# Optimization experiments

Hardware: AMD Instinct MI355X
Metric: run time of the kernel (lower is better)

Reference implementation:

```python
import jax, jax.numpy as jnp
import numpy as np

N, D, E, H, O, K = 4096, 1024, 8, 2048, 1024, 2
LOSS_COEF = 0.01


def setup_inputs() -> dict:
    key = jax.random.key(0)
    ks = jax.random.split(key, 8)
    x = jax.random.normal(ks[0], (N, D), jnp.float32)
    return {
        "x": x,
        "x_offsets": jnp.array([0, N // 2, N], jnp.int32),  # unused by forward math
        "max_seq_len": 2048,
        "group_norm": False,
        "num_groups": 8,
        "linear_dim": D // 8,
        "norm_weight": jax.random.uniform(ks[1], (D,), jnp.float32, 0.5, 1.5),
        "norm_bias": jax.random.normal(ks[2], (D,), jnp.float32) * 0.1,
        "norm_eps": 1e-5,
        "w_gate": jax.random.normal(ks[3], (D, E), jnp.float32) * (1.0 / np.sqrt(D)),
        "experts_hidden_w": jax.random.normal(ks[4], (E, H, D), jnp.float32) * 0.02,
        "experts_hidden_bias": jnp.zeros((E, H), jnp.float32),
        "experts_w": jax.random.normal(ks[5], (E, O, H), jnp.float32) * 0.02,
        "experts_bias": jnp.zeros((E, O), jnp.float32),
        "output_weight": jax.random.normal(ks[6], (D, O), jnp.float32) * 0.02,
    }


def _cv_squared(v, eps=1e-6):
    v = v.astype(jnp.float32)
    m = v.mean()
    return jnp.var(v, ddof=1) / (m * m + eps)  # torch .var() is unbiased


def reference(x, x_offsets, max_seq_len, group_norm, num_groups, linear_dim,
              norm_weight, norm_bias, norm_eps,
              w_gate, experts_hidden_w, experts_hidden_bias,
              experts_w, experts_bias, output_weight):
    # ---- input normalization (layer_norm branch; group_norm=False) ----
    if group_norm:
        xg = x.reshape(-1, num_groups, linear_dim)
        mu = xg.mean(axis=2, keepdims=True)
        var = ((xg - mu) ** 2).mean(axis=2, keepdims=True)
        xg = (xg - mu) * jax.lax.rsqrt(var + norm_eps)
        xg = xg * norm_weight[None, :, None] + norm_bias[None, :, None]
        x_norm = xg.reshape(-1, x.shape[-1])
    else:
        mu = x.mean(axis=-1, keepdims=True)
        var = ((x - mu) ** 2).mean(axis=-1, keepdims=True)  # biased, like F.layer_norm
        x_norm = (x - mu) * jax.lax.rsqrt(var + norm_eps) * norm_weight + norm_bias

    # ---- gating: clean logits (enable_noisy_gating=False), L2-normalize rows ----
    logits = x_norm @ w_gate                                  # [N, E]
    logits = logits / jnp.maximum(
        jnp.linalg.norm(logits, axis=1, keepdims=True), 1e-12)
    probs = jax.nn.softmax(logits, axis=1)                    # softmax over all experts
    _, top_idx = jax.lax.top_k(logits, K)                     # [N, K]
    gates_k = jnp.take_along_axis(probs, top_idx, axis=1)     # top-k of softmax(logits)
    rows = jnp.arange(logits.shape[0])[:, None]
    gates = jnp.zeros_like(logits).at[rows, top_idx].set(gates_k)  # [N, E] sparse gates

    # ---- load-balancing loss (train=True, non-noisy path) ----
    importance = gates.sum(axis=0)
    load = (gates > 0).sum(axis=0).astype(jnp.float32)
    loss = (_cv_squared(importance) + _cv_squared(load)) * LOSS_COEF

    # ---- expert MLPs; gates are exactly zero off top-k so masked-dense == dispatch ----
    h = jax.nn.silu(jnp.einsum('nd,ehd->enh', x_norm, experts_hidden_w)
                    + experts_hidden_bias[:, None, :])        # [E, N, H]
    eo = jnp.einsum('enh,eoh->eno', h, experts_w) + experts_bias[:, None, :]  # [E, N, O]
    y_moe = jnp.einsum('ne,eno->no', gates.astype(jnp.float32),
                       eo.astype(jnp.float32))                # fp32 combine, like index_add

    # ---- residual projection: addmm(y_moe, x, output_weight) ----
    y = y_moe + x @ output_weight
    gate_fraction = load / load.sum()
    return (y, loss, gate_fraction)
```

## Files before the change

### kernel.cpp

```cpp
#include <hip/hip_runtime.h>
#include <hip/hip_bf16.h>
#include <stdint.h>

#define N_TOK 4096
#define DIM   1024
#define NE    8
#define NH    2048
#define NO    1024

typedef __attribute__((ext_vector_type(8))) short bf16x8;
typedef __attribute__((ext_vector_type(16))) float f32x16;

__device__ inline unsigned short f2bf(float f) {
    unsigned u = __float_as_uint(f);
    u += 0x7fffu + ((u >> 16) & 1u);
    return (unsigned short)(u >> 16);
}

__device__ inline void async_copy16(const void* g, void* l) {
    __builtin_amdgcn_global_load_lds(
        (const __attribute__((address_space(1))) void*)g,
        (__attribute__((address_space(3))) void*)l, 16, 0, 0);
}

__global__ __launch_bounds__(256) void ln_gate_kernel(
    const float* __restrict__ x, const float* __restrict__ nw,
    const float* __restrict__ nb, const float* __restrict__ eps_p,
    const float* __restrict__ wg,
    unsigned short* __restrict__ xn_bf, unsigned short* __restrict__ x_bf,
    int* __restrict__ tok_e, float* __restrict__ tok_g)
{
    int n = blockIdx.x;
    int t = threadIdx.x;
    int lane = t & 63, wv = t >> 6;

    const float4 xv = ((const float4*)(x + (size_t)n * DIM))[t];
    float s  = xv.x + xv.y + xv.z + xv.w;
    float s2 = xv.x*xv.x + xv.y*xv.y + xv.z*xv.z + xv.w*xv.w;
    #pragma unroll
    for (int o = 32; o > 0; o >>= 1) {
        s  += __shfl_down(s, o);
        s2 += __shfl_down(s2, o);
    }
    __shared__ float rs[4], rs2[4];
    __shared__ float gred[4][NE];
    if (lane == 0) { rs[wv] = s; rs2[wv] = s2; }
    __syncthreads();
    float S  = rs[0] + rs[1] + rs[2] + rs[3];
    float S2 = rs2[0] + rs2[1] + rs2[2] + rs2[3];
    const float inv = 1.0f / (float)DIM;
    float mu = S * inv;
    float var = fmaxf(S2 * inv - mu * mu, 0.0f);
    float rstd = rsqrtf(var + eps_p[0]);

    float4 w4 = ((const float4*)nw)[t];
    float4 b4 = ((const float4*)nb)[t];
    float xn0 = (xv.x - mu) * rstd * w4.x + b4.x;
    float xn1 = (xv.y - mu) * rstd * w4.y + b4.y;
    float xn2 = (xv.z - mu) * rstd * w4.z + b4.z;
    float xn3 = (xv.w - mu) * rstd * w4.w + b4.w;

    ushort4 pn; pn.x = f2bf(xn0); pn.y = f2bf(xn1); pn.z = f2bf(xn2); pn.w = f2bf(xn3);
    ((ushort4*)(xn_bf + (size_t)n * DIM))[t] = pn;
    ushort4 px; px.x = f2bf(xv.x); px.y = f2bf(xv.y); px.z = f2bf(xv.z); px.w = f2bf(xv.w);
    ((ushort4*)(x_bf + (size_t)n * DIM))[t] = px;

    float acc[NE];
    #pragma unroll
    for (int e = 0; e < NE; ++e) acc[e] = 0.0f;
    float xns[4] = {xn0, xn1, xn2, xn3};
    const float4* wgp = (const float4*)(wg + (size_t)(4 * t) * NE);
    #pragma unroll
    for (int j = 0; j < 4; ++j) {
        float4 w0 = wgp[2 * j], w1 = wgp[2 * j + 1];
        float xj = xns[j];
        acc[0] += xj * w0.x; acc[1] += xj * w0.y; acc[2] += xj * w0.z; acc[3] += xj * w0.w;
        acc[4] += xj * w1.x; acc[5] += xj * w1.y; acc[6] += xj * w1.z; acc[7] += xj * w1.w;
    }
    #pragma unroll
    for (int o = 32; o > 0; o >>= 1) {
        #pragma unroll
        for (int e = 0; e < NE; ++e) acc[e] += __shfl_down(acc[e], o);
    }
    if (lane == 0) {
        #pragma unroll
        for (int e = 0; e < NE; ++e) gred[wv][e] = acc[e];
    }
    __syncthreads();
    if (t == 0) {
        float lg[NE];
        float nrm2 = 0.0f;
        #pragma unroll
        for (int e = 0; e < NE; ++e) {
            lg[e] = gred[0][e] + gred[1][e] + gred[2][e] + gred[3][e];
            nrm2 += lg[e] * lg[e];
        }
        float den = fmaxf(sqrtf(nrm2), 1e-12f);
        float linv = 1.0f / den;
        #pragma unroll
        for (int e = 0; e < NE; ++e) lg[e] *= linv;
        float mx = lg[0];
        #pragma unroll
        for (int e = 1; e < NE; ++e) mx = fmaxf(mx, lg[e]);
        float p[NE], ps = 0.0f;
        #pragma unroll
        for (int e = 0; e < NE; ++e) { p[e] = expf(lg[e] - mx); ps += p[e]; }
        float pinv = 1.0f / ps;
        #pragma unroll
        for (int e = 0; e < NE; ++e) p[e] *= pinv;
        int i0 = 0; float b0 = lg[0];
        #pragma unroll
        for (int e = 1; e < NE; ++e) if (lg[e] > b0) { b0 = lg[e]; i0 = e; }
        int i1 = -1; float b1 = -3.0e38f;
        #pragma unroll
        for (int e = 0; e < NE; ++e) if (e != i0 && lg[e] > b1) { b1 = lg[e]; i1 = e; }
        tok_e[2 * n] = i0; tok_e[2 * n + 1] = i1;
        tok_g[2 * n] = p[i0]; tok_g[2 * n + 1] = p[i1];
    }
}

__device__ inline float cv_sq(const float* v) {
    float m = 0.0f;
    for (int e = 0; e < NE; ++e) m += v[e];
    m *= (1.0f / NE);
    float s = 0.0f;
    for (int e = 0; e < NE; ++e) { float d = v[e] - m; s += d * d; }
    s *= (1.0f / (NE - 1));
    return s / (m * m + 1e-6f);
}

#define CVT_BLK 32768
__global__ __launch_bounds__(256) void prep_kernel(
    const float* __restrict__ whw, unsigned short* __restrict__ wh_bf,
    const float* __restrict__ wow, unsigned short* __restrict__ wo_bf,
    const float* __restrict__ wout, unsigned short* __restrict__ wt_bf,
    const int* __restrict__ tok_e, const float* __restrict__ tok_g,
    int* __restrict__ counts, int* __restrict__ offsets,
    int* __restrict__ rowsbuf, float* __restrict__ gatebuf,
    float* __restrict__ out_tail)
{
    __shared__ float tile[32][33];
    __shared__ int   sc[4][NE], sp[4][NE];
    __shared__ float sf[4][NE];
    __shared__ int   lcur[NE];

    int b = blockIdx.x, t = threadIdx.x;

    if (b < CVT_BLK) {
        const int n4each = NE * NH * DIM / 4;
        int i = b * 256 + t;
        const float4* s; ushort4* d; int j;
        if (i < n4each) { s = (const float4*)whw; d = (ushort4*)wh_bf; j = i; }
        else            { s = (const float4*)wow; d = (ushort4*)wo_bf; j = i - n4each; }
        float4 v = s[j];
        ushort4 o; o.x = f2bf(v.x); o.y = f2bf(v.y); o.z = f2bf(v.z); o.w = f2bf(v.w);
        d[j] = o;
        return;
    }
    if (b < CVT_BLK + 1024) {
        int idx = b - CVT_BLK;
        int o0 = (idx & 31) * 32, d0 = (idx >> 5) * 32;
        int tx = t & 31, ty0 = t >> 5;
        #pragma unroll
        for (int k = 0; k < 4; ++k) {
            int ty = ty0 + k * 8;
            tile[ty][tx] = wout[(size_t)(d0 + ty) * NO + o0 + tx];
        }
        __syncthreads();
        #pragma unroll
        for (int k = 0; k < 4; ++k) {
            int ty = ty0 + k * 8;
            wt_bf[(size_t)(o0 + ty) * DIM + d0 + tx] = f2bf(tile[tx][ty]);
        }
        return;
    }

    int rb = b - (CVT_BLK + 1024);
    int lane = t & 63, wv = t >> 6;
    int chunk0 = rb * 1024;

    int lc[NE]; float li[NE];
    #pragma unroll
    for (int e = 0; e < NE; ++e) { lc[e] = 0; li[e] = 0.0f; }
    int base = t * 32;
    #pragma unroll
    for (int q = 0; q < 8; ++q) {
        int4 e4 = *(const int4*)(tok_e + base + q * 4);
        float4 g4 = *(const float4*)(tok_g + base + q * 4);
        lc[e4.x]++; li[e4.x] += g4.x;
        lc[e4.y]++; li[e4.y] += g4.y;
        lc[e4.z]++; li[e4.z] += g4.z;
        lc[e4.w]++; li[e4.w] += g4.w;
    }
    int prior_flag = (base + 32 <= chunk0) ? 1 : 0;
    int lp[NE];
    #pragma unroll
    for (int e = 0; e < NE; ++e) lp[e] = prior_flag ? lc[e] : 0;

    #pragma unroll
    for (int o = 32; o > 0; o >>= 1) {
        #pragma unroll
        for (int e = 0; e < NE; ++e) {
            lc[e] += __shfl_down(lc[e], o);
            lp[e] += __shfl_down(lp[e], o);
            li[e] += __shfl_down(li[e], o);
        }
    }
    if (lane == 0) {
        #pragma unroll
        for (int e = 0; e < NE; ++e) { sc[wv][e] = lc[e]; sp[wv][e] = lp[e]; sf[wv][e] = li[e]; }
    }
    __syncthreads();
    if (t == 0) {
        int cnt[NE], pri[NE]; float imp[NE];
        for (int e = 0; e < NE; ++e) {
            cnt[e] = sc[0][e] + sc[1][e] + sc[2][e] + sc[3][e];
            pri[e] = sp[0][e] + sp[1][e] + sp[2][e] + sp[3][e];
            imp[e] = sf[0][e] + sf[1][e] + sf[2][e] + sf[3][e];
        }
        int off = 0;
        for (int e = 0; e < NE; ++e) {
            lcur[e] = off + pri[e];
            if (rb == 0) { counts[e] = cnt[e]; offsets[e] = off; }
            off += cnt[e];
        }
        if (rb == 0) {
            float lcf[NE], lif[NE];
            for (int e = 0; e < NE; ++e) { lcf[e] = (float)cnt[e]; lif[e] = imp[e]; }
            float tot = (float)off;
            out_tail[0] = 0.01f * (cv_sq(lif) + cv_sq(lcf));
            for (int e = 0; e < NE; ++e) out_tail[1 + e] = lcf[e] / tot;
        }
    }
    __syncthreads();

    int g0 = chunk0 + 4 * t;
    int4 e4 = *(const int4*)(tok_e + g0);
    float4 g4 = *(const float4*)(tok_g + g0);
    int s0 = atomicAdd(&lcur[e4.x], 1);
    int s1 = atomicAdd(&lcur[e4.y], 1);
    int s2 = atomicAdd(&lcur[e4.z], 1);
    int s3 = atomicAdd(&lcur[e4.w], 1);
    int tok0 = g0 >> 1;
    rowsbuf[s0] = tok0;     rowsbuf[s1] = tok0;
    rowsbuf[s2] = tok0 + 1; rowsbuf[s3] = tok0 + 1;
    gatebuf[s0] = g4.x; gatebuf[s1] = g4.y;
    gatebuf[s2] = g4.z; gatebuf[s3] = g4.w;
}

#define BK 64

__global__ __launch_bounds__(256) void gemm1_kernel(
    const unsigned short* __restrict__ xn,
    const unsigned short* __restrict__ wh,
    const float* __restrict__ hb,
    const int* __restrict__ rowsbuf,
    const int* __restrict__ counts, const int* __restrict__ offsets,
    unsigned short* __restrict__ hbuf)
{
    int e = blockIdx.z;
    int count = counts[e];
    int tm = blockIdx.y, tn = blockIdx.x;
    if (tm * 128 >= count) return;
    int off = offsets[e];

    __shared__ alignas(16) short As[128 * BK];
    __shared__ alignas(16) short Bs[128 * BK];

    int t = threadIdx.x;
    int c = t & 7, rl = t >> 3;
    int csw = (c ^ (rl & 7)) * 8;
    const unsigned short* aptr[4];
    const unsigned short* bptr[4];
    #pragma unroll
    for (int p = 0; p < 4; ++p) {
        int mrow = tm * 128 + p * 32 + rl;
        int mc = mrow < count ? mrow : count - 1;
        int token = rowsbuf[off + mc];
        aptr[p] = xn + (size_t)token * DIM;
        bptr[p] = wh + ((size_t)e * NH + tn * 128 + p * 32 + rl) * DIM;
    }

    int lane = t & 63, wvi = t >> 6;
    int wm = (wvi & 1) * 64, wn = (wvi >> 1) * 64;
    int l31 = lane & 31, h = lane >> 5, sw = l31 & 7;

    f32x16 acc[2][2];
    #pragma unroll
    for (int i = 0; i < 2; ++i)
        #pragma unroll
        for (int j = 0; j < 2; ++j) acc[i][j] = (f32x16)(0.0f);

    for (int kt = 0; kt < DIM / BK; ++kt) {
        int kb = kt * BK + csw;
        #pragma unroll
        for (int p = 0; p < 4; ++p)
            async_copy16(aptr[p] + kb, (char*)As + p * 4096 + t * 16);
        #pragma unroll
        for (int p = 0; p < 4; ++p)
            async_copy16(bptr[p] + kb, (char*)Bs + p * 4096 + t * 16);
        __syncthreads();
        #pragma unroll
        for (int ks = 0; ks < 4; ++ks) {
            int ph = ((ks * 2 + h) ^ sw) * 8;
            bf16x8 af[2], bfr[2];
            #pragma unroll
            for (int i = 0; i < 2; ++i)
                af[i] = *(const bf16x8*)&As[(wm + i * 32 + l31) * BK + ph];
            #pragma unroll
            for (int j = 0; j < 2; ++j)
                bfr[j] = *(const bf16x8*)&Bs[(wn + j * 32 + l31) * BK + ph];
            #pragma unroll
            for (int i = 0; i < 2; ++i)
                #pragma unroll
                for (int j = 0; j < 2; ++j)
                    acc[i][j] = __builtin_amdgcn_mfma_f32_32x32x16_bf16(af[i], bfr[j], acc[i][j], 0, 0, 0);
        }
        __syncthreads();
    }

    #pragma unroll
    for (int i = 0; i < 2; ++i) {
        #pragma unroll
        for (int j = 0; j < 2; ++j) {
            int col = tn * 128 + wn + j * 32 + l31;
            float bias = hb[e * NH + col];
            #pragma unroll
            for (int r = 0; r < 16; ++r) {
                int row_d = (r & 3) + 8 * (r >> 2) + 4 * h;
                int m = tm * 128 + wm + i * 32 + row_d;
                if (m < count) {
                    float v = acc[i][j][r] + bias;
                    v = v / (1.0f + __expf(-v));
                    hbuf[(size_t)(off + m) * NH + col] = f2bf(v);
                }
            }
        }
    }
}

__global__ __launch_bounds__(256) void gemm2_kernel(
    const unsigned short* __restrict__ hbuf,
    const unsigned short* __restrict__ wo,
    const float* __restrict__ ob,
    const int* __restrict__ counts, const int* __restrict__ offsets,
    const int* __restrict__ rowsbuf, const float* __restrict__ gatebuf,
    float* __restrict__ y)
{
    int e = blockIdx.z;
    int count = counts[e];
    int tm = blockIdx.y, tn = blockIdx.x;
    if (tm * 128 >= count) return;
    int off = offsets[e];

    __shared__ alignas(16) short As[128 * BK];
    __shared__ alignas(16) short Bs[64 * BK];

    int t = threadIdx.x;
    int c = t & 7, rl = t >> 3;
    int csw = (c ^ (rl & 7)) * 8;
    const unsigned short* aptr[4];
    const unsigned short* bptr[2];
    #pragma unroll
    for (int p = 0; p < 4; ++p) {
        int mrow = tm * 128 + p * 32 + rl;
        int mc = mrow < count ? mrow : count - 1;
        aptr[p] = hbuf + (size_t)(off + mc) * NH;
    }
    #pragma unroll
    for (int p = 0; p < 2; ++p)
        bptr[p] = wo + ((size_t)e * NO + tn * 64 + p * 32 + rl) * NH;

    int lane = t & 63, wvi = t >> 6;
    int wm = (wvi & 1) * 64, wn = (wvi >> 1) * 32;
    int l31 = lane & 31, h = lane >> 5, sw = l31 & 7;

    f32x16 acc[2];
    #pragma unroll
    for (int i = 0; i < 2; ++i) acc[i] = (f32x16)(0.0f);

    for (int kt = 0; kt < NH / BK; ++kt) {
        int kb = kt * BK + csw;
        #pragma unroll
        for (int p = 0; p < 4; ++p)
            async_copy16(aptr[p] + kb, (char*)As + p * 4096 + t * 16);
        #pragma unroll
        for (int p = 0; p < 2; ++p)
            async_copy16(bptr[p] + kb, (char*)Bs + p * 4096 + t * 16);
        __syncthreads();
        #pragma unroll
        for (int ks = 0; ks < 4; ++ks) {
            int ph = ((ks * 2 + h) ^ sw) * 8;
            bf16x8 af[2], bfr;
            #pragma unroll
            for (int i = 0; i < 2; ++i)
                af[i] = *(const bf16x8*)&As[(wm + i * 32 + l31) * BK + ph];
            bfr = *(const bf16x8*)&Bs[(wn + l31) * BK + ph];
            #pragma unroll
            for (int i = 0; i < 2; ++i)
                acc[i] = __builtin_amdgcn_mfma_f32_32x32x16_bf16(af[i], bfr, acc[i], 0, 0, 0);
        }
        __syncthreads();
    }

    int col = tn * 64 + wn + l31;
    float bias = ob[e * NO + col];
    #pragma unroll
    for (int i = 0; i < 2; ++i) {
        #pragma unroll
        for (int r = 0; r < 16; ++r) {
            int row_d = (r & 3) + 8 * (r >> 2) + 4 * h;
            int m = tm * 128 + wm + i * 32 + row_d;
            if (m < count) {
                int slot = off + m;
                int token = rowsbuf[slot];
                float g = gatebuf[slot];
                __hip_atomic_fetch_add(&y[(size_t)token * NO + col],
                                       g * (acc[i][r] + bias),
                                       __ATOMIC_RELAXED, __HIP_MEMORY_SCOPE_AGENT);
            }
        }
    }
}

__global__ __launch_bounds__(256) void gemm_res_kernel(
    const unsigned short* __restrict__ xb,
    const unsigned short* __restrict__ wt,
    float* __restrict__ y)
{
    int tm = blockIdx.y, tn = blockIdx.x;
    __shared__ alignas(16) short As[64 * BK];
    __shared__ alignas(16) short Bs[128 * BK];

    int t = threadIdx.x;
    int c = t & 7, rl = t >> 3;
    int csw = (c ^ (rl & 7)) * 8;
    const unsigned short* aptr[2];
    const unsigned short* bptr[4];
    #pragma unroll
    for (int p = 0; p < 2; ++p)
        aptr[p] = xb + (size_t)(tm * 64 + p * 32 + rl) * DIM;
    #pragma unroll
    for (int p = 0; p < 4; ++p)
        bptr[p] = wt + (size_t)(tn * 128 + p * 32 + rl) * DIM;

    int lane = t & 63, wvi = t >> 6;
    int wm = (wvi & 1) * 32, wn = (wvi >> 1) * 64;
    int l31 = lane & 31, h = lane >> 5, sw = l31 & 7;

    f32x16 acc[2];
    #pragma unroll
    for (int j = 0; j < 2; ++j) acc[j] = (f32x16)(0.0f);

    for (int kt = 0; kt < DIM / BK; ++kt) {
        int kb = kt * BK + csw;
        #pragma unroll
        for (int p = 0; p < 2; ++p)
            async_copy16(aptr[p] + kb, (char*)As + p * 4096 + t * 16);
        #pragma unroll
        for (int p = 0; p < 4; ++p)
            async_copy16(bptr[p] + kb, (char*)Bs + p * 4096 + t * 16);
        __syncthreads();
        #pragma unroll
        for (int ks = 0; ks < 4; ++ks) {
            int ph = ((ks * 2 + h) ^ sw) * 8;
            bf16x8 af, bfr[2];
            af = *(const bf16x8*)&As[(wm + l31) * BK + ph];
            #pragma unroll
            for (int j = 0; j < 2; ++j)
                bfr[j] = *(const bf16x8*)&Bs[(wn + j * 32 + l31) * BK + ph];
            #pragma unroll
            for (int j = 0; j < 2; ++j)
                acc[j] = __builtin_amdgcn_mfma_f32_32x32x16_bf16(af, bfr[j], acc[j], 0, 0, 0);
        }
        __syncthreads();
    }

    #pragma unroll
    for (int j = 0; j < 2; ++j) {
        int col = tn * 128 + wn + j * 32 + l31;
        #pragma unroll
        for (int r = 0; r < 16; ++r) {
            int row_d = (r & 3) + 8 * (r >> 2) + 4 * h;
            int row = tm * 64 + wm + row_d;
            y[(size_t)row * NO + col] = acc[j][r];
        }
    }
}

extern "C" void kernel_launch(void* const* d_in, const int* in_sizes, int n_in,
                              void* d_out, int out_size, void* d_ws, size_t ws_size,
                              hipStream_t stream) {
    const float* x    = (const float*)d_in[0];
    const float* nw   = (const float*)d_in[6];
    const float* nb   = (const float*)d_in[7];
    const float* eps  = (const float*)d_in[8];
    const float* wg   = (const float*)d_in[9];
    const float* whw  = (const float*)d_in[10];
    const float* whb  = (const float*)d_in[11];
    const float* wow  = (const float*)d_in[12];
    const float* wob  = (const float*)d_in[13];
    const float* wout = (const float*)d_in[14];

    char* ws = (char*)d_ws;
    unsigned short* xn_bf = (unsigned short*)(ws + 0);
    unsigned short* x_bf  = (unsigned short*)(ws + 8388608);
    unsigned short* wh_bf = (unsigned short*)(ws + 16777216);
    unsigned short* wo_bf = (unsigned short*)(ws + 50331648);
    unsigned short* wt_bf = (unsigned short*)(ws + 83886080);
    unsigned short* hbuf  = (unsigned short*)(ws + 85983232);
    char* meta = ws + 119537664;
    int*   counts     = (int*)(meta + 0);
    int*   offsets    = (int*)(meta + 128);
    int*   tok_e      = (int*)(meta + 2048);
    float* tok_g      = (float*)(meta + 2048 + 32768);
    int*   rowsbuf    = (int*)(meta + 2048 + 65536);
    float* gatebuf    = (float*)(meta + 2048 + 98304);

    float* y = (float*)d_out;
    float* out_tail = y + (size_t)N_TOK * NO;

    ln_gate_kernel<<<N_TOK, 256, 0, stream>>>(x, nw, nb, eps, wg, xn_bf, x_bf,
                                              tok_e, tok_g);
    prep_kernel<<<CVT_BLK + 1024 + 8, 256, 0, stream>>>(
        whw, wh_bf, wow, wo_bf, wout, wt_bf,
        tok_e, tok_g, counts, offsets, rowsbuf, gatebuf, out_tail);
    gemm_res_kernel<<<dim3(NO / 128, N_TOK / 64), 256, 0, stream>>>(x_bf, wt_bf, y);
    gemm1_kernel<<<dim3(NH / 128, N_TOK / 128, NE), 256, 0, stream>>>(
        xn_bf, wh_bf, whb, rowsbuf, counts, offsets, hbuf);
    gemm2_kernel<<<dim3(NO / 64, N_TOK / 128, NE), 256, 0, stream>>>(
        hbuf, wo_bf, wob, counts, offsets, rowsbuf, gatebuf, y);
}
```

Baseline: 382.9 us.

## Replace atomic MoE scatter with gather-combine in residual GEMM epilogue

```diff
diff --git a/kernel.cpp b/kernel.cpp
--- a/kernel.cpp
+++ b/kernel.cpp
@@ -23,99 +23,138 @@
         (__attribute__((address_space(3))) void*)l, 16, 0, 0);
 }
 
-__global__ __launch_bounds__(256) void ln_gate_kernel(
+#define LN_BLK  4096
+#define CVT_BLK 32768
+__global__ __launch_bounds__(256) void fused_prep_kernel(
     const float* __restrict__ x, const float* __restrict__ nw,
     const float* __restrict__ nb, const float* __restrict__ eps_p,
     const float* __restrict__ wg,
     unsigned short* __restrict__ xn_bf, unsigned short* __restrict__ x_bf,
-    int* __restrict__ tok_e, float* __restrict__ tok_g)
+    int* __restrict__ tok_e, float* __restrict__ tok_g,
+    const float* __restrict__ whw, unsigned short* __restrict__ wh_bf,
+    const float* __restrict__ wow, unsigned short* __restrict__ wo_bf,
+    const float* __restrict__ wout, unsigned short* __restrict__ wt_bf)
 {
-    int n = blockIdx.x;
-    int t = threadIdx.x;
-    int lane = t & 63, wv = t >> 6;
-
-    const float4 xv = ((const float4*)(x + (size_t)n * DIM))[t];
-    float s  = xv.x + xv.y + xv.z + xv.w;
-    float s2 = xv.x*xv.x + xv.y*xv.y + xv.z*xv.z + xv.w*xv.w;
-    #pragma unroll
-    for (int o = 32; o > 0; o >>= 1) {
-        s  += __shfl_down(s, o);
-        s2 += __shfl_down(s2, o);
-    }
+    __shared__ float tile[32][33];
     __shared__ float rs[4], rs2[4];
     __shared__ float gred[4][NE];
-    if (lane == 0) { rs[wv] = s; rs2[wv] = s2; }
+
+    int b = blockIdx.x, t = threadIdx.x;
+
+    if (b < LN_BLK) {
+        int n = b;
+        int lane = t & 63, wv = t >> 6;
+
+        const float4 xv = ((const float4*)(x + (size_t)n * DIM))[t];
+        float s  = xv.x + xv.y + xv.z + xv.w;
+        float s2 = xv.x*xv.x + xv.y*xv.y + xv.z*xv.z + xv.w*xv.w;
+        #pragma unroll
+        for (int o = 32; o > 0; o >>= 1) {
+            s  += __shfl_down(s, o);
+            s2 += __shfl_down(s2, o);
+        }
+        if (lane == 0) { rs[wv] = s; rs2[wv] = s2; }
+        __syncthreads();
+        float S  = rs[0] + rs[1] + rs[2] + rs[3];
+        float S2 = rs2[0] + rs2[1] + rs2[2] + rs2[3];
+        const float inv = 1.0f / (float)DIM;
+        float mu = S * inv;
+        float var = fmaxf(S2 * inv - mu * mu, 0.0f);
+        float rstd = rsqrtf(var + eps_p[0]);
+
+        float4 w4 = ((const float4*)nw)[t];
+        float4 b4 = ((const float4*)nb)[t];
+        float xn0 = (xv.x - mu) * rstd * w4.x + b4.x;
+        float xn1 = (xv.y - mu) * rstd * w4.y + b4.y;
+        float xn2 = (xv.z - mu) * rstd * w4.z + b4.z;
+        float xn3 = (xv.w - mu) * rstd * w4.w + b4.w;
+
+        ushort4 pn; pn.x = f2bf(xn0); pn.y = f2bf(xn1); pn.z = f2bf(xn2); pn.w = f2bf(xn3);
+        ((ushort4*)(xn_bf + (size_t)n * DIM))[t] = pn;
+        ushort4 px; px.x = f2bf(xv.x); px.y = f2bf(xv.y); px.z = f2bf(xv.z); px.w = f2bf(xv.w);
+        ((ushort4*)(x_bf + (size_t)n * DIM))[t] = px;
+
+        float acc[NE];
+        #pragma unroll
+        for (int e = 0; e < NE; ++e) acc[e] = 0.0f;
+        float xns[4] = {xn0, xn1, xn2, xn3};
+        const float4* wgp = (const float4*)(wg + (size_t)(4 * t) * NE);
+        #pragma unroll
+        for (int j = 0; j < 4; ++j) {
+            float4 w0 = wgp[2 * j], w1 = wgp[2 * j + 1];
+            float xj = xns[j];
+            acc[0] += xj * w0.x; acc[1] += xj * w0.y; acc[2] += xj * w0.z; acc[3] += xj * w0.w;
+            acc[4] += xj * w1.x; acc[5] += xj * w1.y; acc[6] += xj * w1.z; acc[7] += xj * w1.w;
+        }
+        #pragma unroll
+        for (int o = 32; o > 0; o >>= 1) {
+            #pragma unroll
+            for (int e = 0; e < NE; ++e) acc[e] += __shfl_down(acc[e], o);
+        }
+        if (lane == 0) {
+            #pragma unroll
+            for (int e = 0; e < NE; ++e) gred[wv][e] = acc[e];
+        }
+        __syncthreads();
+        if (t == 0) {
+            float lg[NE];
+            float nrm2 = 0.0f;
+            #pragma unroll
+            for (int e = 0; e < NE; ++e) {
+                lg[e] = gred[0][e] + gred[1][e] + gred[2][e] + gred[3][e];
+                nrm2 += lg[e] * lg[e];
+            }
+            float den = fmaxf(sqrtf(nrm2), 1e-12f);
+            float linv = 1.0f / den;
+            #pragma unroll
+            for (int e = 0; e < NE; ++e) lg[e] *= linv;
+            float mx = lg[0];
+            #pragma unroll
+            for (int e = 1; e < NE; ++e) mx = fmaxf(mx, lg[e]);
+            float p[NE], ps = 0.0f;
+            #pragma unroll
+            for (int e = 0; e < NE; ++e) { p[e] = expf(lg[e] - mx); ps += p[e]; }
+            float pinv = 1.0f / ps;
+            #pragma unroll
+            for (int e = 0; e < NE; ++e) p[e] *= pinv;
+            int i0 = 0; float b0 = lg[0];
+            #pragma unroll
+            for (int e = 1; e < NE; ++e) if (lg[e] > b0) { b0 = lg[e]; i0 = e; }
+            int i1 = -1; float b1 = -3.0e38f;
+            #pragma unroll
+            for (int e = 0; e < NE; ++e) if (e != i0 && lg[e] > b1) { b1 = lg[e]; i1 = e; }
+            tok_e[2 * n] = i0; tok_e[2 * n + 1] = i1;
+            tok_g[2 * n] = p[i0]; tok_g[2 * n + 1] = p[i1];
+        }
+        return;
+    }
+
+    int b2 = b - LN_BLK;
+    if (b2 < CVT_BLK) {
+        const int n4each = NE * NH * DIM / 4;
+        int i = b2 * 256 + t;
+        const float4* s; ushort4* d; int j;
+        if (i < n4each) { s = (const float4*)whw; d = (ushort4*)wh_bf; j = i; }
+        else            { s = (const float4*)wow; d = (ushort4*)wo_bf; j = i - n4each; }
+        float4 v = s[j];
+        ushort4 o; o.x = f2bf(v.x); o.y = f2bf(v.y); o.z = f2bf(v.z); o.w = f2bf(v.w);
+        d[j] = o;
+        return;
+    }
+
+    int idx = b2 - CVT_BLK;
+    int o0 = (idx & 31) * 32, d0 = (idx >> 5) * 32;
+    int tx = t & 31, ty0 = t >> 5;
+    #pragma unroll
+    for (int k = 0; k < 4; ++k) {
+        int ty = ty0 + k * 8;
+        tile[ty][tx] = wout[(size_t)(d0 + ty) * NO + o0 + tx];
+    }
     __syncthreads();
-    float S  = rs[0] + rs[1] + rs[2] + rs[3];
-    float S2 = rs2[0] + rs2[1] + rs2[2] + rs2[3];
-    const float inv = 1.0f / (float)DIM;
-    float mu = S * inv;
-    float var = fmaxf(S2 * inv - mu * mu, 0.0f);
-    float rstd = rsqrtf(var + eps_p[0]);
-
-    float4 w4 = ((const float4*)nw)[t];
-    float4 b4 = ((const float4*)nb)[t];
-    float xn0 = (xv.x - mu) * rstd * w4.x + b4.x;
-    float xn1 = (xv.y - mu) * rstd * w4.y + b4.y;
-    float xn2 = (xv.z - mu) * rstd * w4.z + b4.z;
-    float xn3 = (xv.w - mu) * rstd * w4.w + b4.w;
-
-    ushort4 pn; pn.x = f2bf(xn0); pn.y = f2bf(xn1); pn.z = f2bf(xn2); pn.w = f2bf(xn3);
-    ((ushort4*)(xn_bf + (size_t)n * DIM))[t] = pn;
-    ushort4 px; px.x = f2bf(xv.x); px.y = f2bf(xv.y); px.z = f2bf(xv.z); px.w = f2bf(xv.w);
-    ((ushort4*)(x_bf + (size_t)n * DIM))[t] = px;
-
-    float acc[NE];
-    #pragma unroll
-    for (int e = 0; e < NE; ++e) acc[e] = 0.0f;
-    float xns[4] = {xn0, xn1, xn2, xn3};
-    const float4* wgp = (const float4*)(wg + (size_t)(4 * t) * NE);
-    #pragma unroll
-    for (int j = 0; j < 4; ++j) {
-        float4 w0 = wgp[2 * j], w1 = wgp[2 * j + 1];
-        float xj = xns[j];
-        acc[0] += xj * w0.x; acc[1] += xj * w0.y; acc[2] += xj * w0.z; acc[3] += xj * w0.w;
-        acc[4] += xj * w1.x; acc[5] += xj * w1.y; acc[6] += xj * w1.z; acc[7] += xj * w1.w;
-    }
-    #pragma unroll
-    for (int o = 32; o > 0; o >>= 1) {
-        #pragma unroll
-        for (int e = 0; e < NE; ++e) acc[e] += __shfl_down(acc[e], o);
-    }
-    if (lane == 0) {
-        #pragma unroll
-        for (int e = 0; e < NE; ++e) gred[wv][e] = acc[e];
-    }
-    __syncthreads();
-    if (t == 0) {
-        float lg[NE];
-        float nrm2 = 0.0f;
-        #pragma unroll
-        for (int e = 0; e < NE; ++e) {
-            lg[e] = gred[0][e] + gred[1][e] + gred[2][e] + gred[3][e];
-            nrm2 += lg[e] * lg[e];
-        }
-        float den = fmaxf(sqrtf(nrm2), 1e-12f);
-        float linv = 1.0f / den;
-        #pragma unroll
-        for (int e = 0; e < NE; ++e) lg[e] *= linv;
-        float mx = lg[0];
-        #pragma unroll
-        for (int e = 1; e < NE; ++e) mx = fmaxf(mx, lg[e]);
-        float p[NE], ps = 0.0f;
-        #pragma unroll
-        for (int e = 0; e < NE; ++e) { p[e] = expf(lg[e] - mx); ps += p[e]; }
-        float pinv = 1.0f / ps;
-        #pragma unroll
-        for (int e = 0; e < NE; ++e) p[e] *= pinv;
-        int i0 = 0; float b0 = lg[0];
-        #pragma unroll
-        for (int e = 1; e < NE; ++e) if (lg[e] > b0) { b0 = lg[e]; i0 = e; }
-        int i1 = -1; float b1 = -3.0e38f;
-        #pragma unroll
-        for (int e = 0; e < NE; ++e) if (e != i0 && lg[e] > b1) { b1 = lg[e]; i1 = e; }
-        tok_e[2 * n] = i0; tok_e[2 * n + 1] = i1;
-        tok_g[2 * n] = p[i0]; tok_g[2 * n + 1] = p[i1];
+    #pragma unroll
+    for (int k = 0; k < 4; ++k) {
+        int ty = ty0 + k * 8;
+        wt_bf[(size_t)(o0 + ty) * DIM + d0 + tx] = f2bf(tile[tx][ty]);
     }
 }
 
@@ -129,53 +168,17 @@
     return s / (m * m + 1e-6f);
 }
 
-#define CVT_BLK 32768
-__global__ __launch_bounds__(256) void prep_kernel(
-    const float* __restrict__ whw, unsigned short* __restrict__ wh_bf,
-    const float* __restrict__ wow, unsigned short* __restrict__ wo_bf,
-    const float* __restrict__ wout, unsigned short* __restrict__ wt_bf,
+__global__ __launch_bounds__(256) void routing_kernel(
     const int* __restrict__ tok_e, const float* __restrict__ tok_g,
     int* __restrict__ counts, int* __restrict__ offsets,
-    int* __restrict__ rowsbuf, float* __restrict__ gatebuf,
+    int* __restrict__ rowsbuf, int* __restrict__ invslot,
     float* __restrict__ out_tail)
 {
-    __shared__ float tile[32][33];
     __shared__ int   sc[4][NE], sp[4][NE];
     __shared__ float sf[4][NE];
     __shared__ int   lcur[NE];
 
-    int b = blockIdx.x, t = threadIdx.x;
-
-    if (b < CVT_BLK) {
-        const int n4each = NE * NH * DIM / 4;
-        int i = b * 256 + t;
-        const float4* s; ushort4* d; int j;
-        if (i < n4each) { s = (const float4*)whw; d = (ushort4*)wh_bf; j = i; }
-        else            { s = (const float4*)wow; d = (ushort4*)wo_bf; j = i - n4each; }
-        float4 v = s[j];
-        ushort4 o; o.x = f2bf(v.x); o.y = f2bf(v.y); o.z = f2bf(v.z); o.w = f2bf(v.w);
-        d[j] = o;
-        return;
-    }
-    if (b < CVT_BLK + 1024) {
-        int idx = b - CVT_BLK;
-        int o0 = (idx & 31) * 32, d0 = (idx >> 5) * 32;
-        int tx = t & 31, ty0 = t >> 5;
-        #pragma unroll
-        for (int k = 0; k < 4; ++k) {
-            int ty = ty0 + k * 8;
-            tile[ty][tx] = wout[(size_t)(d0 + ty) * NO + o0 + tx];
-        }
-        __syncthreads();
-        #pragma unroll
-        for (int k = 0; k < 4; ++k) {
-            int ty = ty0 + k * 8;
-            wt_bf[(size_t)(o0 + ty) * DIM + d0 + tx] = f2bf(tile[tx][ty]);
-        }
-        return;
-    }
-
-    int rb = b - (CVT_BLK + 1024);
+    int rb = blockIdx.x, t = threadIdx.x;
     int lane = t & 63, wv = t >> 6;
     int chunk0 = rb * 1024;
 
@@ -236,7 +239,6 @@
 
     int g0 = chunk0 + 4 * t;
     int4 e4 = *(const int4*)(tok_e + g0);
-    float4 g4 = *(const float4*)(tok_g + g0);
     int s0 = atomicAdd(&lcur[e4.x], 1);
     int s1 = atomicAdd(&lcur[e4.y], 1);
     int s2 = atomicAdd(&lcur[e4.z], 1);
@@ -244,8 +246,8 @@
     int tok0 = g0 >> 1;
     rowsbuf[s0] = tok0;     rowsbuf[s1] = tok0;
     rowsbuf[s2] = tok0 + 1; rowsbuf[s3] = tok0 + 1;
-    gatebuf[s0] = g4.x; gatebuf[s1] = g4.y;
-    gatebuf[s2] = g4.z; gatebuf[s3] = g4.w;
+    invslot[g0]     = s0;   invslot[g0 + 1] = s1;
+    invslot[g0 + 2] = s2;   invslot[g0 + 3] = s3;
 }
 
 #define BK 64
@@ -344,8 +346,7 @@
     const unsigned short* __restrict__ wo,
     const float* __restrict__ ob,
     const int* __restrict__ counts, const int* __restrict__ offsets,
-    const int* __restrict__ rowsbuf, const float* __restrict__ gatebuf,
-    float* __restrict__ y)
+    float* __restrict__ eo)
 {
     int e = blockIdx.z;
     int count = counts[e];
@@ -354,30 +355,30 @@
     int off = offsets[e];
 
     __shared__ alignas(16) short As[128 * BK];
-    __shared__ alignas(16) short Bs[64 * BK];
+    __shared__ alignas(16) short Bs[128 * BK];
 
     int t = threadIdx.x;
     int c = t & 7, rl = t >> 3;
     int csw = (c ^ (rl & 7)) * 8;
     const unsigned short* aptr[4];
-    const unsigned short* bptr[2];
+    const unsigned short* bptr[4];
     #pragma unroll
     for (int p = 0; p < 4; ++p) {
         int mrow = tm * 128 + p * 32 + rl;
         int mc = mrow < count ? mrow : count - 1;
         aptr[p] = hbuf + (size_t)(off + mc) * NH;
-    }
-    #pragma unroll
-    for (int p = 0; p < 2; ++p)
-        bptr[p] = wo + ((size_t)e * NO + tn * 64 + p * 32 + rl) * NH;
+        bptr[p] = wo + ((size_t)e * NO + tn * 128 + p * 32 + rl) * NH;
+    }
 
     int lane = t & 63, wvi = t >> 6;
-    int wm = (wvi & 1) * 64, wn = (wvi >> 1) * 32;
+    int wm = (wvi & 1) * 64, wn = (wvi >> 1) * 64;
     int l31 = lane & 31, h = lane >> 5, sw = l31 & 7;
 
-    f32x16 acc[2];
-    #pragma unroll
-    for (int i = 0; i < 2; ++i) acc[i] = (f32x16)(0.0f);
+    f32x16 acc[2][2];
+    #pragma unroll
+    for (int i = 0; i < 2; ++i)
+        #pragma unroll
+        for (int j = 0; j < 2; ++j) acc[i][j] = (f32x16)(0.0f);
 
     for (int kt = 0; kt < NH / BK; ++kt) {
         int kb = kt * BK + csw;
@@ -385,39 +386,40 @@
         for (int p = 0; p < 4; ++p)
             async_copy16(aptr[p] + kb, (char*)As + p * 4096 + t * 16);
         #pragma unroll
-        for (int p = 0; p < 2; ++p)
+        for (int p = 0; p < 4; ++p)
             async_copy16(bptr[p] + kb, (char*)Bs + p * 4096 + t * 16);
         __syncthreads();
         #pragma unroll
         for (int ks = 0; ks < 4; ++ks) {
             int ph = ((ks * 2 + h) ^ sw) * 8;
-            bf16x8 af[2], bfr;
+            bf16x8 af[2], bfr[2];
             #pragma unroll
             for (int i = 0; i < 2; ++i)
                 af[i] = *(const bf16x8*)&As[(wm + i * 32 + l31) * BK + ph];
-            bfr = *(const bf16x8*)&Bs[(wn + l31) * BK + ph];
+            #pragma unroll
+            for (int j = 0; j < 2; ++j)
+                bfr[j] = *(const bf16x8*)&Bs[(wn + j * 32 + l31) * BK + ph];
             #pragma unroll
             for (int i = 0; i < 2; ++i)
-                acc[i] = __builtin_amdgcn_mfma_f32_32x32x16_bf16(af[i], bfr, acc[i], 0, 0, 0);
-        }
-        __syncthreads();
-    }
-
-    int col = tn * 64 + wn + l31;
-    float bias = ob[e * NO + col];
+                #pragma unroll
+                for (int j = 0; j < 2; ++j)
+                    acc[i][j] = __builtin_amdgcn_mfma_f32_32x32x16_bf16(af[i], bfr[j], acc[i][j], 0, 0, 0);
+        }
+        __syncthreads();
+    }
+
     #pragma unroll
     for (int i = 0; i < 2; ++i) {
         #pragma unroll
-        for (int r = 0; r < 16; ++r) {
-            int row_d = (r & 3) + 8 * (r >> 2) + 4 * h;
-            int m = tm * 128 + wm + i * 32 + row_d;
-            if (m < count) {
-                int slot = off + m;
-                int token = rowsbuf[slot];
-                float g = gatebuf[slot];
-                __hip_atomic_fetch_add(&y[(size_t)token * NO + col],
-                                       g * (acc[i][r] + bias),
-                                       __ATOMIC_RELAXED, __HIP_MEMORY_SCOPE_AGENT);
+        for (int j = 0; j < 2; ++j) {
+            int col = tn * 128 + wn + j * 32 + l31;
+            float bias = ob[e * NO + col];
+            #pragma unroll
+            for (int r = 0; r < 16; ++r) {
+                int row_d = (r & 3) + 8 * (r >> 2) + 4 * h;
+                int m = tm * 128 + wm + i * 32 + row_d;
+                if (m < count)
+                    eo[(size_t)(off + m) * NO + col] = acc[i][j][r] + bias;
             }
         }
     }
@@ -426,6 +428,9 @@
 __global__ __launch_bounds__(256) void gemm_res_kernel(
     const unsigned short* __restrict__ xb,
     const unsigned short* __restrict__ wt,
+    const float* __restrict__ eo,
+    const int* __restrict__ invslot,
+    const float* __restrict__ tok_g,
     float* __restrict__ y)
 {
     int tm = blockIdx.y, tn = blockIdx.x;
@@ -477,13 +482,17 @@
     }
 
     #pragma unroll
-    for (int j = 0; j < 2; ++j) {
-        int col = tn * 128 + wn + j * 32 + l31;
-        #pragma unroll
-        for (int r = 0; r < 16; ++r) {
-            int row_d = (r & 3) + 8 * (r >> 2) + 4 * h;
-            int row = tm * 64 + wm + row_d;
-            y[(size_t)row * NO + col] = acc[j][r];
+    for (int r = 0; r < 16; ++r) {
+        int row_d = (r & 3) + 8 * (r >> 2) + 4 * h;
+        int row = tm * 64 + wm + row_d;
+        int s0 = invslot[2 * row], s1 = invslot[2 * row + 1];
+        float g0 = tok_g[2 * row], g1 = tok_g[2 * row + 1];
+        #pragma unroll
+        for (int j = 0; j < 2; ++j) {
+            int col = tn * 128 + wn + j * 32 + l31;
+            y[(size_t)row * NO + col] = acc[j][r]
+                + g0 * eo[(size_t)s0 * NO + col]
+                + g1 * eo[(size_t)s1 * NO + col];
         }
     }
 }
@@ -509,25 +518,27 @@
     unsigned short* wo_bf = (unsigned short*)(ws + 50331648);
     unsigned short* wt_bf = (unsigned short*)(ws + 83886080);
     unsigned short* hbuf  = (unsigned short*)(ws + 85983232);
+    float* eo = (float*)(ws + 16777216);
     char* meta = ws + 119537664;
     int*   counts     = (int*)(meta + 0);
     int*   offsets    = (int*)(meta + 128);
     int*   tok_e      = (int*)(meta + 2048);
     float* tok_g      = (float*)(meta + 2048 + 32768);
     int*   rowsbuf    = (int*)(meta + 2048 + 65536);
-    float* gatebuf    = (float*)(meta + 2048 + 98304);
+    int*   invslot    = (int*)(meta + 2048 + 98304);
 
     float* y = (float*)d_out;
     float* out_tail = y + (size_t)N_TOK * NO;
 
-    ln_gate_kernel<<<N_TOK, 256, 0, stream>>>(x, nw, nb, eps, wg, xn_bf, x_bf,
-                                              tok_e, tok_g);
-    prep_kernel<<<CVT_BLK + 1024 + 8, 256, 0, stream>>>(
-        whw, wh_bf, wow, wo_bf, wout, wt_bf,
-        tok_e, tok_g, counts, offsets, rowsbuf, gatebuf, out_tail);
-    gemm_res_kernel<<<dim3(NO / 128, N_TOK / 64), 256, 0, stream>>>(x_bf, wt_bf, y);
+    fused_prep_kernel<<<LN_BLK + CVT_BLK + 1024, 256, 0, stream>>>(
+        x, nw, nb, eps, wg, xn_bf, x_bf, tok_e, tok_g,
+        whw, wh_bf, wow, wo_bf, wout, wt_bf);
+    routing_kernel<<<8, 256, 0, stream>>>(
+        tok_e, tok_g, counts, offsets, rowsbuf, invslot, out_tail);
     gemm1_kernel<<<dim3(NH / 128, N_TOK / 128, NE), 256, 0, stream>>>(
         xn_bf, wh_bf, whb, rowsbuf, counts, offsets, hbuf);
-    gemm2_kernel<<<dim3(NO / 64, N_TOK / 128, NE), 256, 0, stream>>>(
-        hbuf, wo_bf, wob, counts, offsets, rowsbuf, gatebuf, y);
-}
+    gemm2_kernel<<<dim3(NO / 128, N_TOK / 128, NE), 256, 0, stream>>>(
+        hbuf, wo_bf, wob, counts, offsets, eo);
+    gemm_res_kernel<<<dim3(NO / 128, N_TOK / 64), 256, 0, stream>>>(
+        x_bf, wt_bf, eo, invslot, tok_g, y);
+}
```

Result: faster. 362.6 us (-5.3%).
